# Kernel tuning notes

Measured on AMD Instinct MI355X. Metric: run time of the kernel, lower is better.

## Reference

```python
import jax, jax.numpy as jnp
import numpy as np

L, D_MODEL, D_INNER, DT_RANK, D_STATE, D_CONV, VOCAB = 4, 768, 1536, 48, 16, 4, 32000
B, S = 1, 1024


def rmsnorm(x, w, eps=1e-5):
    return x * jax.lax.rsqrt(jnp.mean(x * x, axis=-1, keepdims=True) + eps) * w


def causal_depthwise_conv(x, w, b):
    # x: [B,S,D]; w: [D,1,K] (torch Conv1d groups=D weight layout); causal left-pad K-1
    y = jax.lax.conv_general_dilated(
        x.transpose(0, 2, 1), w, window_strides=(1,), padding=[(D_CONV - 1, 0)],
        dimension_numbers=('NCH', 'OIH', 'NCH'), feature_group_count=D_INNER)
    return y.transpose(0, 2, 1) + b


def selective_scan(u, dt, A, Bm, Cm, Dv):
    # Faithful to the source: A_delta = exp(dt (x) A), clamp(min=-20) is a no-op on exp output
    A_delta = jnp.clip(jnp.exp(jnp.einsum('bld,dn->bldn', dt, A)), -20.0, None)
    B_delta_u = jnp.einsum('bld,bld,bln->bldn', dt, u, Bm)
    shifted = jnp.pad(A_delta[:, 1:], ((0, 0), (1, 0), (0, 0), (0, 0)))
    A_cum = jnp.exp(jnp.cumsum(shifted, axis=1))
    h = B_delta_u / (A_cum + 1e-12)
    y = jnp.einsum('bldn,bln->bld', jnp.cumsum(h, axis=1) * A_cum, Cm)
    return y + u * Dv


def setup_inputs() -> dict:
    key = jax.random.key(0)
    ks = jax.random.split(key, 8)
    return {
        'tokens': jax.random.randint(ks[0], (B, S), 0, VOCAB),
        'embedding': jax.random.normal(ks[1], (VOCAB, D_MODEL), jnp.float32) * 0.02,
        'norm_w': jnp.ones((L, D_MODEL), jnp.float32),
        'in_proj_w': jax.random.normal(ks[2], (L, 2 * D_INNER, D_MODEL), jnp.float32) * 0.02,
        'conv_w': jax.random.normal(ks[3], (L, D_INNER, 1, D_CONV), jnp.float32) * 0.2,
        'conv_b': jnp.zeros((L, D_INNER), jnp.float32),
        'x_proj_w': jax.random.normal(ks[4], (L, DT_RANK + 2 * D_STATE, D_INNER), jnp.float32) * 0.02,
        'dt_proj_w': jax.random.normal(ks[5], (L, D_INNER, DT_RANK), jnp.float32) * 0.001,
        'dt_proj_b': jnp.full((L, D_INNER), 5.0, jnp.float32),  # delta~5 keeps exp(cumsum(exp(dt*A))) finite
        'A_log': jnp.tile(jnp.log(jnp.arange(1, D_STATE + 1, dtype=jnp.float32)), (L, D_INNER, 1)),
        'D_skip': jnp.ones((L, D_INNER), jnp.float32),
        'out_proj_w': jax.random.normal(ks[6], (L, D_MODEL, D_INNER), jnp.float32) * 0.02,
        'final_norm_w': jnp.ones((D_MODEL,), jnp.float32),
    }


def reference(tokens, embedding, norm_w, in_proj_w, conv_w, conv_b, x_proj_w,
              dt_proj_w, dt_proj_b, A_log, D_skip, out_proj_w, final_norm_w):
    x = embedding[tokens]  # [B,S,d_model]
    for i in range(L):
        h = rmsnorm(x, norm_w[i])
        xz = h @ in_proj_w[i].T                      # [B,S,2*d_inner]
        xi, res = xz[..., :D_INNER], xz[..., D_INNER:]
        xi = jax.nn.silu(causal_depthwise_conv(xi, conv_w[i], conv_b[i]))
        proj = xi @ x_proj_w[i].T                    # [B,S,dt_rank+2*d_state]
        dt = jax.nn.softplus(proj[..., :DT_RANK] @ dt_proj_w[i].T + dt_proj_b[i])
        Bm = proj[..., DT_RANK:DT_RANK + D_STATE]
        Cm = proj[..., DT_RANK + D_STATE:]
        A = -jnp.exp(A_log[i])                       # [d_inner, d_state]
        y = selective_scan(xi, dt, A, Bm, Cm, D_skip[i])
        x = x + (y * jax.nn.silu(res)) @ out_proj_w[i].T
    return rmsnorm(x, final_norm_w) @ embedding.T    # tied LM head: [B,S,vocab]
```

## Files before the change

### kernel.cpp

```cpp
#include <hip/hip_runtime.h>
#include <hip/hip_bf16.h>
#include <cmath>

namespace {

constexpr int kL      = 4;
constexpr int kDModel = 768;
constexpr int kDInner = 1536;
constexpr int kDtRank = 48;
constexpr int kDState = 16;
constexpr int kDConv  = 4;
constexpr int kSeq    = 1024;
constexpr int kPLd    = 96;
constexpr int kPB     = 128;
constexpr int kVocab  = 32000;
constexpr int kCH     = 64;
constexpr int kNCH    = kSeq / kCH;
constexpr int kDN     = kDInner * kDState;
constexpr int kSplitIn  = 4;
constexpr int kSplitOut = 8;

using short8 = __attribute__((ext_vector_type(8))) short;
using f32x4  = __attribute__((ext_vector_type(4))) float;

__device__ __forceinline__ float silu_f(float v) {
    return v / (1.f + __expf(-v));
}

__device__ __forceinline__ unsigned short f2bu(float v) {
    __hip_bfloat16 h = __float2bfloat16(v);
    return *reinterpret_cast<unsigned short*>(&h);
}

__device__ __forceinline__ void split_bf16(float v, __hip_bfloat16& hi, __hip_bfloat16& lo) {
    hi = __float2bfloat16(v);
    lo = __float2bfloat16(v - __bfloat162float(hi));
}

__device__ __forceinline__ void split_u(float v, unsigned short& hi, unsigned short& lo) {
    __hip_bfloat16 h, l;
    split_bf16(v, h, l);
    hi = *reinterpret_cast<unsigned short*>(&h);
    lo = *reinterpret_cast<unsigned short*>(&l);
}

__global__ void __launch_bounds__(256) f2b_kernel(
    const float* __restrict__ src, __hip_bfloat16* __restrict__ dst, int n) {
    int i = (blockIdx.x * 256 + threadIdx.x) * 8;
    const int stride = gridDim.x * 256 * 8;
    for (; i + 7 < n; i += stride) {
        const float4 a = *reinterpret_cast<const float4*>(src + i);
        const float4 b = *reinterpret_cast<const float4*>(src + i + 4);
        union { unsigned short u[8]; uint4 v; } pk;
        pk.u[0] = f2bu(a.x); pk.u[1] = f2bu(a.y); pk.u[2] = f2bu(a.z); pk.u[3] = f2bu(a.w);
        pk.u[4] = f2bu(b.x); pk.u[5] = f2bu(b.y); pk.u[6] = f2bu(b.z); pk.u[7] = f2bu(b.w);
        *reinterpret_cast<uint4*>(reinterpret_cast<unsigned short*>(dst) + i) = pk.v;
    }
}

__global__ void __launch_bounds__(256) split3_kernel(
    const float* __restrict__ src, int rows, int cols,
    __hip_bfloat16* __restrict__ dst) {
    const int idx = blockIdx.x * 256 + threadIdx.x;
    const int c4cnt = cols >> 2;
    if (idx >= rows * c4cnt) return;
    const int r = idx / c4cnt, c = (idx % c4cnt) << 2;
    const float4 v = *reinterpret_cast<const float4*>(src + (size_t)r * cols + c);
    ushort4 hi4, lo4;
    split_u(v.x, hi4.x, lo4.x); split_u(v.y, hi4.y, lo4.y);
    split_u(v.z, hi4.z, lo4.z); split_u(v.w, hi4.w, lo4.w);
    unsigned short* row = reinterpret_cast<unsigned short*>(dst) + (size_t)r * 3 * cols;
    *reinterpret_cast<ushort4*>(row + c) = hi4;
    *reinterpret_cast<ushort4*>(row + cols + c) = hi4;
    *reinterpret_cast<ushort4*>(row + 2 * cols + c) = lo4;
}

__global__ void __launch_bounds__(256) dup2_kernel(
    const float* __restrict__ src, __hip_bfloat16* __restrict__ dst,
    int rows, int cols) {
    const int idx = blockIdx.x * 256 + threadIdx.x;
    const int c4cnt = cols >> 2;
    if (idx >= rows * c4cnt) return;
    const int r = idx / c4cnt, c = (idx % c4cnt) << 2;
    const float4 v = *reinterpret_cast<const float4*>(src + (size_t)r * cols + c);
    ushort4 hi4 = {f2bu(v.x), f2bu(v.y), f2bu(v.z), f2bu(v.w)};
    unsigned short* row = reinterpret_cast<unsigned short*>(dst) + (size_t)r * 2 * cols;
    *reinterpret_cast<ushort4*>(row + c) = hi4;
    *reinterpret_cast<ushort4*>(row + cols + c) = hi4;
}

__global__ void __launch_bounds__(256) split3x_kernel(
    const float* __restrict__ src, __hip_bfloat16* __restrict__ dst) {
    const int idx = blockIdx.x * 256 + threadIdx.x;
    constexpr int c4cnt = kDInner >> 2;
    if (idx >= kL * kPB * c4cnt) return;
    const int layer = idx / (kPB * c4cnt);
    const int rem   = idx % (kPB * c4cnt);
    const int r = rem / c4cnt, c = (rem % c4cnt) << 2;
    float4 v = {0.f, 0.f, 0.f, 0.f};
    if (r < kDtRank + 2 * kDState)
        v = *reinterpret_cast<const float4*>(
            src + (size_t)layer * (kDtRank + 2 * kDState) * kDInner + (size_t)r * kDInner + c);
    ushort4 hi4, lo4;
    split_u(v.x, hi4.x, lo4.x); split_u(v.y, hi4.y, lo4.y);
    split_u(v.z, hi4.z, lo4.z); split_u(v.w, hi4.w, lo4.w);
    unsigned short* row = reinterpret_cast<unsigned short*>(dst)
        + ((size_t)layer * kPB + r) * 3 * kDInner;
    *reinterpret_cast<ushort4*>(row + c) = hi4;
    *reinterpret_cast<ushort4*>(row + kDInner + c) = hi4;
    *reinterpret_cast<ushort4*>(row + 2 * kDInner + c) = lo4;
}

__global__ void __launch_bounds__(256) embed_rms_kernel(
    const int* __restrict__ tokens, const float* __restrict__ emb,
    const float* __restrict__ w, float* __restrict__ x,
    __hip_bfloat16* __restrict__ h2) {
    const int s = blockIdx.x;
    const int t = tokens[s];
    const float* src = emb + (size_t)t * kDModel;
    float v[3];
    float ss = 0.f;
    #pragma unroll
    for (int j = 0; j < 3; ++j) {
        const int d = threadIdx.x + j * 256;
        v[j] = src[d];
        x[(size_t)s * kDModel + d] = v[j];
        ss = fmaf(v[j], v[j], ss);
    }
    #pragma unroll
    for (int m = 32; m; m >>= 1) ss += __shfl_xor(ss, m);
    __shared__ float red[4];
    if ((threadIdx.x & 63) == 0) red[threadIdx.x >> 6] = ss;
    __syncthreads();
    const float total = red[0] + red[1] + red[2] + red[3];
    const float scale = rsqrtf(total / (float)kDModel + 1e-5f);
    __hip_bfloat16* dst = h2 + (size_t)s * 3 * kDModel;
    #pragma unroll
    for (int j = 0; j < 3; ++j) {
        const int d = threadIdx.x + j * 256;
        const float hv = v[j] * scale * w[d];
        __hip_bfloat16 hi, lo;
        split_bf16(hv, hi, lo);
        dst[d] = hi; dst[kDModel + d] = lo; dst[2 * kDModel + d] = hi;
    }
}

template <bool FINAL>
__global__ void __launch_bounds__(256) reduce_rms_kernel(
    const float* __restrict__ parts, size_t stride,
    const float* __restrict__ w, float* __restrict__ x,
    __hip_bfloat16* __restrict__ out) {
    const int s = blockIdx.x;
    float v[3];
    float ss = 0.f;
    #pragma unroll
    for (int j = 0; j < 3; ++j) {
        const int d = threadIdx.x + j * 256;
        const size_t off = (size_t)s * kDModel + d;
        float acc = x[off];
        #pragma unroll
        for (int p = 0; p < kSplitOut; ++p) acc += parts[(size_t)p * stride + off];
        v[j] = acc;
        x[off] = acc;
        ss = fmaf(acc, acc, ss);
    }
    #pragma unroll
    for (int m = 32; m; m >>= 1) ss += __shfl_xor(ss, m);
    __shared__ float red[4];
    if ((threadIdx.x & 63) == 0) red[threadIdx.x >> 6] = ss;
    __syncthreads();
    const float total = red[0] + red[1] + red[2] + red[3];
    const float scale = rsqrtf(total / (float)kDModel + 1e-5f);
    #pragma unroll
    for (int j = 0; j < 3; ++j) {
        const int d = threadIdx.x + j * 256;
        const float hv = v[j] * scale * w[d];
        if (FINAL) {
            out[(size_t)s * kDModel + d] = __float2bfloat16(hv);
        } else {
            __hip_bfloat16 hi, lo;
            split_bf16(hv, hi, lo);
            __hip_bfloat16* dst = out + (size_t)s * 3 * kDModel;
            dst[d] = hi; dst[kDModel + d] = lo; dst[2 * kDModel + d] = hi;
        }
    }
}

template <int BM, int BN, int KSPLIT>
__global__ void __launch_bounds__(256) mfma_gemm(
    const __hip_bfloat16* __restrict__ A, int lda,
    const __hip_bfloat16* __restrict__ B, int ldb,
    float* __restrict__ C, int ldc,
    int N, int K, size_t partStride) {
    constexpr int BK = 32;
    static_assert(BM == 128 && BN == 128, "staging assumes 128x128");
    __shared__ unsigned short As[2][BM * BK];
    __shared__ unsigned short Bs[2][BN * BK];
    const int tid  = threadIdx.x;
    const int lane = tid & 63;

    const int nwg = gridDim.x * gridDim.y;
    int bid = blockIdx.y * gridDim.x + blockIdx.x;
    {
        const int q = nwg >> 3, r = nwg & 7;
        const int xcd = bid & 7, pos = bid >> 3;
        bid = (xcd < r ? xcd * (q + 1) : r * (q + 1) + (xcd - r) * q) + pos;
    }
    const int m0 = (bid % gridDim.x) * BM;
    const int n0 = (bid / gridDim.x) * BN;

    const int Kp = K / KSPLIT;
    const int kbeg = (KSPLIT > 1) ? blockIdx.z * Kp : 0;
    float* Cw = (KSPLIT > 1) ? C + (size_t)blockIdx.z * partStride : C;
    constexpr int WM = BM / 2, WN = BN / 2;
    constexpr int MR = WM / 16, NR = WN / 16;
    const int wave = tid >> 6;
    const int wm = (wave >> 1) * WM, wn = (wave & 1) * WN;
    const int l15 = lane & 15, l4 = lane >> 4;
    f32x4 acc[MR][NR] = {};

    auto stage = [&](int buf, int k0) {
        #pragma unroll
        for (int i = 0; i < 2; ++i) {
            const int idx = tid + i * 256;
            const int r = idx >> 2, qv = idx & 3;
            const int qs = qv ^ ((r >> 1) & 3);
            __builtin_amdgcn_global_load_lds(
                (const __attribute__((address_space(1))) void*)(A + (size_t)(m0 + r) * lda + k0 + qs * 8),
                (__attribute__((address_space(3))) void*)(&As[buf][(idx - lane) * 8]),
                16, 0, 0);
        }
        #pragma unroll
        for (int i = 0; i < 2; ++i) {
            const int idx = tid + i * 256;
            const int r = idx >> 2, qv = idx & 3;
            const int qs = qv ^ ((r >> 1) & 3);
            __builtin_amdgcn_global_load_lds(
                (const __attribute__((address_space(1))) void*)(B + (size_t)(n0 + r) * ldb + k0 + qs * 8),
                (__attribute__((address_space(3))) void*)(&Bs[buf][(idx - lane) * 8]),
                16, 0, 0);
        }
    };

    const int nt = Kp / BK;
    int cur = 0;
    stage(0, kbeg);
    for (int t = 0; t < nt; ++t) {
        if (t + 1 < nt) {
            stage(cur ^ 1, kbeg + (t + 1) * BK);
            asm volatile("s_waitcnt vmcnt(4)" ::: "memory");
        } else {
            asm volatile("s_waitcnt vmcnt(0)" ::: "memory");
        }
        __builtin_amdgcn_s_barrier();

        short8 af[MR], bfv[NR];
        #pragma unroll
        for (int mi = 0; mi < MR; ++mi) {
            const int R = wm + mi * 16 + l15;
            af[mi] = *reinterpret_cast<const short8*>(&As[cur][(R * 4 + (l4 ^ ((R >> 1) & 3))) * 8]);
        }
        #pragma unroll
        for (int ni = 0; ni < NR; ++ni) {
            const int R = wn + ni * 16 + l15;
            bfv[ni] = *reinterpret_cast<const short8*>(&Bs[cur][(R * 4 + (l4 ^ ((R >> 1) & 3))) * 8]);
        }
        #pragma unroll
        for (int mi = 0; mi < MR; ++mi)
            #pragma unroll
            for (int ni = 0; ni < NR; ++ni)
                acc[mi][ni] = __builtin_amdgcn_mfma_f32_16x16x32_bf16(
                    af[mi], bfv[ni], acc[mi][ni], 0, 0, 0);

        asm volatile("s_waitcnt lgkmcnt(0)" ::: "memory");
        __builtin_amdgcn_s_barrier();
        cur ^= 1;
    }

    #pragma unroll
    for (int mi = 0; mi < MR; ++mi) {
        const int mrow = m0 + wm + mi * 16 + l4 * 4;
        #pragma unroll
        for (int ni = 0; ni < NR; ++ni) {
            const int ncol = n0 + wn + ni * 16 + l15;
            if (ncol >= N) continue;
            #pragma unroll
            for (int r = 0; r < 4; ++r)
                Cw[(size_t)(mrow + r) * ldc + ncol] = acc[mi][ni][r];
        }
    }
}

template <int NP>
__global__ void __launch_bounds__(256) reduce_parts(
    const float* __restrict__ parts, size_t stride,
    float* __restrict__ dst, int count) {
    const int i = (blockIdx.x * 256 + threadIdx.x) * 4;
    if (i >= count) return;
    float4 s = *reinterpret_cast<const float4*>(parts + i);
    #pragma unroll
    for (int p = 1; p < NP; ++p) {
        const float4 v = *reinterpret_cast<const float4*>(parts + (size_t)p * stride + i);
        s.x += v.x; s.y += v.y; s.z += v.z; s.w += v.w;
    }
    *reinterpret_cast<float4*>(dst + i) = s;
}

__global__ void __launch_bounds__(256) conv_silu_kernel(
    const float* __restrict__ parts, size_t stride,
    const float* __restrict__ cw, const float* __restrict__ cb,
    float* __restrict__ xi, __hip_bfloat16* __restrict__ xi2) {
    const int s = blockIdx.x;
    const int d = blockIdx.y * 256 + threadIdx.x;
    float acc = cb[d];
    #pragma unroll
    for (int k = 0; k < kDConv; ++k) {
        const int sl = s - (kDConv - 1) + k;
        if (sl >= 0) {
            const size_t off = (size_t)sl * (2 * kDInner) + d;
            float xzv = parts[off];
            #pragma unroll
            for (int p = 1; p < kSplitIn; ++p) xzv += parts[(size_t)p * stride + off];
            acc = fmaf(xzv, cw[d * kDConv + k], acc);
        }
    }
    const float v = silu_f(acc);
    xi[(size_t)s * kDInner + d] = v;
    __hip_bfloat16 hi, lo;
    split_bf16(v, hi, lo);
    __hip_bfloat16* row = xi2 + (size_t)s * 3 * kDInner;
    row[d] = hi; row[kDInner + d] = lo; row[2 * kDInner + d] = hi;
}


__device__ __forceinline__ void compute_dt_tile(
    const float* __restrict__ proj, const float* __restrict__ dtw,
    const float* __restrict__ dtb, int l0, int d0, int tid,
    float (*sP)[kDtRank], float (*sdtw)[kDtRank + 1], float (*sdt)[16]) {
    for (int idx = tid; idx < kCH * kDtRank; idx += 256) {
        const int r = idx / kDtRank, c = idx % kDtRank;
        sP[r][c] = proj[(size_t)(l0 + r) * kPLd + c];
    }
    for (int idx = tid; idx < 16 * kDtRank; idx += 256) {
        const int dd = idx / kDtRank, c = idx % kDtRank;
        sdtw[dd][c] = dtw[(size_t)(d0 + dd) * kDtRank + c];
    }
    __syncthreads();
    #pragma unroll
    for (int e = 0; e < 4; ++e) {
        const int idx = tid + e * 256;
        const int r = idx >> 4, dd = idx & 15;
        float acc = dtb[d0 + dd];
        #pragma unroll
        for (int k = 0; k < kDtRank; ++k)
            acc = fmaf(sP[r][k], sdtw[dd][k], acc);
        acc = (acc > 20.f) ? acc : log1pf(__expf(acc));
        sdt[r][dd] = acc;
    }
}

__global__ void __launch_bounds__(256) scan_part1(
    const float* __restrict__ u, const float* __restrict__ proj,
    const float* __restrict__ A_log, const float* __restrict__ dtw,
    const float* __restrict__ dtb,
    float* __restrict__ P, float* __restrict__ S) {
    __shared__ float sP[kCH][kDtRank];
    __shared__ float sdtw[16][kDtRank + 1];
    __shared__ float sdt[kCH][16], su[kCH][16], sB[kCH][16];
    const int tid = threadIdx.x;
    const int n = tid & 15, dl = tid >> 4;
    const int d0 = blockIdx.x * 16;
    const int l0 = blockIdx.y * kCH;
    for (int idx = tid; idx < kCH * 16; idx += 256) {
        const int r = idx >> 4, c = idx & 15;
        su[r][c] = u[(size_t)(l0 + r) * kDInner + d0 + c];
        sB[r][c] = proj[(size_t)(l0 + r) * kPLd + kDtRank + c];
    }
    compute_dt_tile(proj, dtw, dtb, l0, d0, tid, sP, sdtw, sdt);
    __syncthreads();
    const int d = d0 + dl;
    const float Adn = -__expf(A_log[d * kDState + n]);
    float state = 0.f, sumA = 0.f;
    #pragma unroll 8
    for (int l = 0; l < kCH; ++l) {
        const float dtv = sdt[l][dl];
        const float adelta = __expf(dtv * Adn);
        const float mult = __expf(adelta);
        state = fmaf(state, mult, dtv * su[l][dl] * sB[l][n]);
        sumA += adelta;
    }
    const int dn = d * kDState + n;
    P[(size_t)blockIdx.y * kDN + dn] = __expf(sumA);
    S[(size_t)blockIdx.y * kDN + dn] = state;
}

__global__ void __launch_bounds__(256) scan_part2(
    const float* __restrict__ u, const float* __restrict__ proj,
    const float* __restrict__ A_log, const float* __restrict__ dtw,
    const float* __restrict__ dtb, const float* __restrict__ D_skip,
    const float* __restrict__ P, const float* __restrict__ S,
    const float* __restrict__ resparts, size_t rstride,
    __hip_bfloat16* __restrict__ g2) {
    __shared__ float sP[kCH][kDtRank];
    __shared__ float sdtw[16][kDtRank + 1];
    __shared__ float sdt[kCH][16], su[kCH][16], sB[kCH][16], sC[kCH][16];
    __shared__ float sy[kCH][16];
    const int tid = threadIdx.x;
    const int n = tid & 15, dl = tid >> 4;
    const int d0 = blockIdx.x * 16;
    const int l0 = blockIdx.y * kCH;
    for (int idx = tid; idx < kCH * 16; idx += 256) {
        const int r = idx >> 4, c = idx & 15;
        su[r][c] = u[(size_t)(l0 + r) * kDInner + d0 + c];
        sB[r][c] = proj[(size_t)(l0 + r) * kPLd + kDtRank + c];
        sC[r][c] = proj[(size_t)(l0 + r) * kPLd + kDtRank + kDState + c];
    }
    compute_dt_tile(proj, dtw, dtb, l0, d0, tid, sP, sdtw, sdt);
    const int dn = d0 * kDState + tid;
    float state = 0.f;
    for (int jj = 0; jj < (int)blockIdx.y; ++jj) {
        const size_t idx = (size_t)jj * kDN + dn;
        state = fmaf(state, P[idx], S[idx]);
    }
    __syncthreads();
    const int d = d0 + dl;
    const float Adn = -__expf(A_log[d * kDState + n]);
    const float Dv  = D_skip[d];
    for (int l = 0; l < kCH; ++l) {
        const float dtv = sdt[l][dl];
        const float uv  = su[l][dl];
        const float mult = __expf(__expf(dtv * Adn));
        state = fmaf(state, mult, dtv * uv * sB[l][n]);
        float contrib = state * sC[l][n];
        contrib += __shfl_xor(contrib, 8);
        contrib += __shfl_xor(contrib, 4);
        contrib += __shfl_xor(contrib, 2);
        contrib += __shfl_xor(contrib, 1);
        if (n == 0) sy[l][dl] = fmaf(uv, Dv, contrib);
    }
    __syncthreads();
    for (int idx = tid; idx < kCH * 16; idx += 256) {
        const int r = idx >> 4, c = idx & 15;
        const size_t roff = (size_t)(l0 + r) * (2 * kDInner) + kDInner + d0 + c;
        float res = resparts[roff];
        #pragma unroll
        for (int p = 1; p < kSplitIn; ++p) res += resparts[(size_t)p * rstride + roff];
        const float v = sy[r][c] * silu_f(res);
        __hip_bfloat16 hi, lo;
        split_bf16(v, hi, lo);
        __hip_bfloat16* row = g2 + (size_t)(l0 + r) * 2 * kDInner;
        row[d0 + c] = hi; row[kDInner + d0 + c] = lo;
    }
}

}

extern "C" void kernel_launch(void* const* d_in, const int* in_sizes, int n_in,
                              void* d_out, int out_size, void* d_ws, size_t ws_size,
                              hipStream_t stream) {
    const int*   tokens       = (const int*)d_in[0];
    const float* embedding    = (const float*)d_in[1];
    const float* norm_w       = (const float*)d_in[2];
    const float* in_proj_w    = (const float*)d_in[3];
    const float* conv_w       = (const float*)d_in[4];
    const float* conv_b       = (const float*)d_in[5];
    const float* x_proj_w     = (const float*)d_in[6];
    const float* dt_proj_w    = (const float*)d_in[7];
    const float* dt_proj_b    = (const float*)d_in[8];
    const float* A_log        = (const float*)d_in[9];
    const float* D_skip       = (const float*)d_in[10];
    const float* out_proj_w   = (const float*)d_in[11];
    const float* final_norm_w = (const float*)d_in[12];
    float* out = (float*)d_out;

    constexpr int K3m = 3 * kDModel;
    constexpr int K3i = 3 * kDInner;
    constexpr int K2i = 2 * kDInner;

    char* ws = (char*)d_ws;
    auto alloc = [&](size_t bytes) { char* p = ws; ws += (bytes + 255) & ~(size_t)255; return p; };
    float* x    = (float*)alloc((size_t)kSeq * kDModel * 4);
    float* xi   = (float*)alloc((size_t)kSeq * kDInner * 4);
    float* proj = (float*)alloc((size_t)kSeq * kPLd * 4);
    float* scanP  = (float*)alloc((size_t)kNCH * kDN * 4);
    float* scanS  = (float*)alloc((size_t)kNCH * kDN * 4);
    float* partsXZ = (float*)alloc((size_t)kSplitIn * kSeq * 2 * kDInner * 4);
    float* partsP  = (float*)alloc((size_t)24 * kSeq * kPLd * 4);
    float* partsO  = (float*)alloc((size_t)kSplitOut * kSeq * kDModel * 4);
    __hip_bfloat16* h_bf   = (__hip_bfloat16*)alloc((size_t)kSeq * kDModel * 2);
    __hip_bfloat16* h2     = (__hip_bfloat16*)alloc((size_t)kSeq * K3m * 2);
    __hip_bfloat16* xi2    = (__hip_bfloat16*)alloc((size_t)kSeq * K3i * 2);
    __hip_bfloat16* g2     = (__hip_bfloat16*)alloc((size_t)kSeq * K2i * 2);
    __hip_bfloat16* emb_bf = (__hip_bfloat16*)alloc((size_t)kVocab * kDModel * 2);
    __hip_bfloat16* inw2   = (__hip_bfloat16*)alloc((size_t)kL * 2 * kDInner * K3m * 2);
    __hip_bfloat16* outw2  = (__hip_bfloat16*)alloc((size_t)kL * kDModel * K2i * 2);
    __hip_bfloat16* xw2    = (__hip_bfloat16*)alloc((size_t)kL * kPB * K3i * 2);

    f2b_kernel<<<4096, 256, 0, stream>>>(embedding, emb_bf, kVocab * kDModel);
    dup2_kernel<<<(kL * kDModel * kDInner / 4 + 255) / 256, 256, 0, stream>>>(
        out_proj_w, outw2, kL * kDModel, kDInner);
    split3_kernel<<<(kL * 2 * kDInner * kDModel / 4 + 255) / 256, 256, 0, stream>>>(
        in_proj_w, kL * 2 * kDInner, kDModel, inw2);
    split3x_kernel<<<(kL * kPB * kDInner / 4 + 255) / 256, 256, 0, stream>>>(
        x_proj_w, xw2);

    embed_rms_kernel<<<kSeq, 256, 0, stream>>>(tokens, embedding, norm_w, x, h2);

    for (int i = 0; i < kL; ++i) {
        mfma_gemm<128, 128, kSplitIn><<<dim3(kSeq / 128, 2 * kDInner / 128, kSplitIn), 256, 0, stream>>>(
            h2, K3m, inw2 + (size_t)i * 2 * kDInner * K3m, K3m,
            partsXZ, 2 * kDInner, 2 * kDInner, K3m, (size_t)kSeq * 2 * kDInner);

        conv_silu_kernel<<<dim3(kSeq, kDInner / 256), 256, 0, stream>>>(
            partsXZ, (size_t)kSeq * 2 * kDInner,
            conv_w + (size_t)i * kDInner * kDConv, conv_b + (size_t)i * kDInner,
            xi, xi2);

        mfma_gemm<128, 128, 24><<<dim3(kSeq / 128, 1, 24), 256, 0, stream>>>(
            xi2, K3i, xw2 + (size_t)i * kPB * K3i, K3i,
            partsP, kPLd, kPLd, K3i, (size_t)kSeq * kPLd);
        reduce_parts<24><<<(kSeq * kPLd / 4 + 255) / 256, 256, 0, stream>>>(
            partsP, (size_t)kSeq * kPLd, proj, kSeq * kPLd);

        const float* A_l  = A_log + (size_t)i * kDInner * kDState;
        const float* dtw  = dt_proj_w + (size_t)i * kDInner * kDtRank;
        const float* dtb  = dt_proj_b + (size_t)i * kDInner;
        scan_part1<<<dim3(kDInner / 16, kNCH), 256, 0, stream>>>(
            xi, proj, A_l, dtw, dtb, scanP, scanS);
        scan_part2<<<dim3(kDInner / 16, kNCH), 256, 0, stream>>>(
            xi, proj, A_l, dtw, dtb, D_skip + (size_t)i * kDInner,
            scanP, scanS, partsXZ, (size_t)kSeq * 2 * kDInner, g2);

        mfma_gemm<128, 128, kSplitOut><<<dim3(kSeq / 128, kDModel / 128, kSplitOut), 256, 0, stream>>>(
            g2, K2i, outw2 + (size_t)i * kDModel * K2i, K2i,
            partsO, kDModel, kDModel, K2i, (size_t)kSeq * kDModel);

        if (i + 1 < kL) {
            reduce_rms_kernel<false><<<kSeq, 256, 0, stream>>>(
                partsO, (size_t)kSeq * kDModel, norm_w + (size_t)(i + 1) * kDModel, x, h2);
        } else {
            reduce_rms_kernel<true><<<kSeq, 256, 0, stream>>>(
                partsO, (size_t)kSeq * kDModel, final_norm_w, x, h_bf);
        }
    }

    mfma_gemm<128, 128, 1><<<dim3(kSeq / 128, kVocab / 128, 1), 256, 0, stream>>>(
        h_bf, kDModel, emb_bf, kDModel, out, kVocab, kVocab, kDModel, 0);
}
```

Before: 767.6 us.

## Add dedicated 256x256 MFMA kernel for the vocab LM-head GEMM

Replaces the generic 128x128 MFMA GEMM for the final 1024x32000x768 LM-head projection with a specialised 256x256-tile, 512-thread kernel. It stages A and B into LDS with direct global-to-LDS loads, an XOR swizzle and double buffering, and interleaves fragment loads with MFMA quadrants under raised wave priority. Workgroup IDs are remapped so that tiles are grouped per XCD for better L2 locality. The larger tiles cut the global traffic per FLOP, but they need 128 KB of dynamic LDS and 128 accumulator floats per thread, which limits occupancy to one block per CU.

```diff
diff --git a/kernel.cpp b/kernel.cpp
--- a/kernel.cpp
+++ b/kernel.cpp
@@ -291,6 +291,129 @@
     }
 }
 
+__global__ void __launch_bounds__(512) vocab_gemm(
+    const __hip_bfloat16* __restrict__ A,
+    const __hip_bfloat16* __restrict__ B,
+    float* __restrict__ C) {
+    constexpr int BM = 256, BN = 256, BK = 64;
+    constexpr int K = kDModel, NT = K / BK;
+    constexpr int lda = kDModel, ldb = kDModel, ldc = kVocab;
+    extern __shared__ unsigned short lds[];
+    unsigned short* AsB = lds;
+    unsigned short* BsB = lds + 2 * BM * BK;
+    const int tid = threadIdx.x, lane = tid & 63;
+    const int wave = tid >> 6;
+    const int wr = wave >> 2;
+    const int wc = wave & 3;
+    const int l15 = lane & 15, l4 = lane >> 4;
+
+    const int nwg = gridDim.x * gridDim.y;
+    int bid = blockIdx.y * gridDim.x + blockIdx.x;
+    {
+        const int q = nwg >> 3, r = nwg & 7;
+        const int xcd = bid & 7, pos = bid >> 3;
+        bid = (xcd < r ? xcd * (q + 1) : r * (q + 1) + (xcd - r) * q) + pos;
+    }
+    const int m0 = (bid % gridDim.x) * BM;
+    const int n0 = (bid / gridDim.x) * BN;
+
+    f32x4 acc[8][4] = {};
+
+    auto stage = [&](int buf, int k0) {
+        #pragma unroll
+        for (int i = 0; i < 4; ++i) {
+            const int idx = tid + i * 512;
+            const int r = idx >> 3, p = idx & 7;
+            const int ps = p ^ (r & 7);
+            __builtin_amdgcn_global_load_lds(
+                (const __attribute__((address_space(1))) void*)(A + (size_t)(m0 + r) * lda + k0 + ps * 8),
+                (__attribute__((address_space(3))) void*)(AsB + (size_t)buf * BM * BK + (size_t)(idx - lane) * 8),
+                16, 0, 0);
+        }
+        #pragma unroll
+        for (int i = 0; i < 4; ++i) {
+            const int idx = tid + i * 512;
+            const int r = idx >> 3, p = idx & 7;
+            const int ps = p ^ (r & 7);
+            __builtin_amdgcn_global_load_lds(
+                (const __attribute__((address_space(1))) void*)(B + (size_t)(n0 + r) * ldb + k0 + ps * 8),
+                (__attribute__((address_space(3))) void*)(BsB + (size_t)buf * BN * BK + (size_t)(idx - lane) * 8),
+                16, 0, 0);
+        }
+    };
+
+    stage(0, 0);
+    for (int t = 0; t < NT; ++t) {
+        asm volatile("s_waitcnt vmcnt(0)" ::: "memory");
+        __builtin_amdgcn_s_barrier();
+        if (t + 1 < NT) stage((t + 1) & 1, (t + 1) * BK);
+        const unsigned short* Ab = AsB + (size_t)(t & 1) * BM * BK;
+        const unsigned short* Bb = BsB + (size_t)(t & 1) * BN * BK;
+
+        short8 af[4][2], bfv[2][2];
+
+#define LOAD_A(MQ)                                                          \
+        _Pragma("unroll")                                                   \
+        for (int mi = 0; mi < 4; ++mi) {                                    \
+            _Pragma("unroll")                                               \
+            for (int kk = 0; kk < 2; ++kk) {                                \
+                const int R = wr * 128 + (MQ) * 64 + mi * 16 + l15;         \
+                const int ps = (kk * 4 + l4) ^ (R & 7);                     \
+                af[mi][kk] = *reinterpret_cast<const short8*>(              \
+                    Ab + ((size_t)R * 8 + ps) * 8);                         \
+            }                                                               \
+        }
+#define LOAD_B(NQ)                                                          \
+        _Pragma("unroll")                                                   \
+        for (int ni = 0; ni < 2; ++ni) {                                    \
+            _Pragma("unroll")                                               \
+            for (int kk = 0; kk < 2; ++kk) {                                \
+                const int R = wc * 64 + (NQ) * 32 + ni * 16 + l15;          \
+                const int ps = (kk * 4 + l4) ^ (R & 7);                     \
+                bfv[ni][kk] = *reinterpret_cast<const short8*>(             \
+                    Bb + ((size_t)R * 8 + ps) * 8);                         \
+            }                                                               \
+        }
+#define QUAD(MQ, NQ)                                                        \
+        __builtin_amdgcn_s_setprio(1);                                      \
+        _Pragma("unroll")                                                   \
+        for (int mi = 0; mi < 4; ++mi)                                      \
+            _Pragma("unroll")                                               \
+            for (int ni = 0; ni < 2; ++ni)                                  \
+                _Pragma("unroll")                                           \
+                for (int kk = 0; kk < 2; ++kk)                              \
+                    acc[(MQ) * 4 + mi][(NQ) * 2 + ni] =                     \
+                        __builtin_amdgcn_mfma_f32_16x16x32_bf16(            \
+                            af[mi][kk], bfv[ni][kk],                        \
+                            acc[(MQ) * 4 + mi][(NQ) * 2 + ni], 0, 0, 0);    \
+        __builtin_amdgcn_s_setprio(0);
+
+        LOAD_A(0); LOAD_B(0);
+        QUAD(0, 0);
+        LOAD_B(1);
+        QUAD(0, 1);
+        LOAD_A(1);
+        QUAD(1, 1);
+        LOAD_B(0);
+        QUAD(1, 0);
+#undef LOAD_A
+#undef LOAD_B
+#undef QUAD
+    }
+
+    #pragma unroll
+    for (int mg = 0; mg < 8; ++mg) {
+        const int mrow = m0 + wr * 128 + mg * 16 + l4 * 4;
+        #pragma unroll
+        for (int ng = 0; ng < 4; ++ng) {
+            const int ncol = n0 + wc * 64 + ng * 16 + l15;
+            #pragma unroll
+            for (int r = 0; r < 4; ++r)
+                C[(size_t)(mrow + r) * ldc + ncol] = acc[mg][ng][r];
+        }
+    }
+}
+
 template <int NP>
 __global__ void __launch_bounds__(256) reduce_parts(
     const float* __restrict__ parts, size_t stride,
@@ -331,7 +454,6 @@
     __hip_bfloat16* row = xi2 + (size_t)s * 3 * kDInner;
     row[d] = hi; row[kDInner + d] = lo; row[2 * kDInner + d] = hi;
 }
-
 
 __device__ __forceinline__ void compute_dt_tile(
     const float* __restrict__ proj, const float* __restrict__ dtw,
@@ -477,6 +599,9 @@
     constexpr int K3i = 3 * kDInner;
     constexpr int K2i = 2 * kDInner;
 
+    (void)hipFuncSetAttribute((const void*)vocab_gemm,
+                              hipFuncAttributeMaxDynamicSharedMemorySize, 131072);
+
     char* ws = (char*)d_ws;
     auto alloc = [&](size_t bytes) { char* p = ws; ws += (bytes + 255) & ~(size_t)255; return p; };
     float* x    = (float*)alloc((size_t)kSeq * kDModel * 4);
@@ -544,6 +669,6 @@
         }
     }
 
-    mfma_gemm<128, 128, 1><<<dim3(kSeq / 128, kVocab / 128, 1), 256, 0, stream>>>(
-        h_bf, kDModel, emb_bf, kDModel, out, kVocab, kVocab, kDModel, 0);
-}
+    vocab_gemm<<<dim3(kSeq / 256, kVocab / 256), 512, 131072, stream>>>(
+        h_bf, emb_bf, out);
+}
```

Measured after the change: 746.1 us. 2.8% less time.

## Merge prep kernels into one launch and add large-tile LM-head GEMM

Applied to the files above, without the earlier changes.

Merges the five preprocessing kernels (embedding bf16 cast, weight duplicate/split, and embed+RMSnorm) into one prep_kernel that dispatches on block index, removing four launches. Replaces the generic 128x128 vocab projection with a dedicated 512x256-tile, 512-thread GEMM. The new GEMM uses triple-buffered global_load_lds staging with XOR swizzling, XCD-aware block remapping and raised wave priority around the MFMAs. Larger tiles cut redundant operand traffic for the biggest GEMM. The cost is heavy register use (64 accumulators per lane), 144KB of LDS, and only 250 workgroups, which may underfill the GPU.

```diff
diff --git a/kernel.cpp b/kernel.cpp
--- a/kernel.cpp
+++ b/kernel.cpp
@@ -20,6 +20,13 @@
 constexpr int kSplitIn  = 4;
 constexpr int kSplitOut = 8;
 
+constexpr int kPrepEmbed   = kSeq;
+constexpr int kPrepF2b     = kVocab * kDModel / (8 * 256);
+constexpr int kPrepDup2    = kL * kDModel * (kDInner / 4) / 256;
+constexpr int kPrepSplit3  = kL * 2 * kDInner * (kDModel / 4) / 256;
+constexpr int kPrepSplit3x = kL * kPB * (kDInner / 4) / 256;
+constexpr int kPrepBlocks  = kPrepEmbed + kPrepF2b + kPrepDup2 + kPrepSplit3 + kPrepSplit3x;
+
 using short8 = __attribute__((ext_vector_type(8))) short;
 using f32x4  = __attribute__((ext_vector_type(4))) float;
 
@@ -44,104 +51,108 @@
     lo = *reinterpret_cast<unsigned short*>(&l);
 }
 
-__global__ void __launch_bounds__(256) f2b_kernel(
-    const float* __restrict__ src, __hip_bfloat16* __restrict__ dst, int n) {
-    int i = (blockIdx.x * 256 + threadIdx.x) * 8;
-    const int stride = gridDim.x * 256 * 8;
-    for (; i + 7 < n; i += stride) {
-        const float4 a = *reinterpret_cast<const float4*>(src + i);
-        const float4 b = *reinterpret_cast<const float4*>(src + i + 4);
+__global__ void __launch_bounds__(256) prep_kernel(
+    const int* __restrict__ tokens, const float* __restrict__ embedding,
+    const float* __restrict__ norm_w, const float* __restrict__ in_proj_w,
+    const float* __restrict__ out_proj_w, const float* __restrict__ x_proj_w,
+    float* __restrict__ x, __hip_bfloat16* __restrict__ h2,
+    __hip_bfloat16* __restrict__ emb_bf, __hip_bfloat16* __restrict__ inw2,
+    __hip_bfloat16* __restrict__ outw2, __hip_bfloat16* __restrict__ xw2) {
+    const int tid = threadIdx.x;
+    int b = blockIdx.x;
+
+    if (b < kPrepEmbed) {
+        const int s = b;
+        const int t = tokens[s];
+        const float* src = embedding + (size_t)t * kDModel;
+        float v[3];
+        float ss = 0.f;
+        #pragma unroll
+        for (int j = 0; j < 3; ++j) {
+            const int d = tid + j * 256;
+            v[j] = src[d];
+            x[(size_t)s * kDModel + d] = v[j];
+            ss = fmaf(v[j], v[j], ss);
+        }
+        #pragma unroll
+        for (int m = 32; m; m >>= 1) ss += __shfl_xor(ss, m);
+        __shared__ float red[4];
+        if ((tid & 63) == 0) red[tid >> 6] = ss;
+        __syncthreads();
+        const float total = red[0] + red[1] + red[2] + red[3];
+        const float scale = rsqrtf(total / (float)kDModel + 1e-5f);
+        __hip_bfloat16* dst = h2 + (size_t)s * 3 * kDModel;
+        #pragma unroll
+        for (int j = 0; j < 3; ++j) {
+            const int d = tid + j * 256;
+            const float hv = v[j] * scale * norm_w[d];
+            __hip_bfloat16 hi, lo;
+            split_bf16(hv, hi, lo);
+            dst[d] = hi; dst[kDModel + d] = lo; dst[2 * kDModel + d] = hi;
+        }
+        return;
+    }
+    b -= kPrepEmbed;
+
+    if (b < kPrepF2b) {
+        const int i = (b * 256 + tid) * 8;
+        const float4 a = *reinterpret_cast<const float4*>(embedding + i);
+        const float4 c = *reinterpret_cast<const float4*>(embedding + i + 4);
         union { unsigned short u[8]; uint4 v; } pk;
         pk.u[0] = f2bu(a.x); pk.u[1] = f2bu(a.y); pk.u[2] = f2bu(a.z); pk.u[3] = f2bu(a.w);
-        pk.u[4] = f2bu(b.x); pk.u[5] = f2bu(b.y); pk.u[6] = f2bu(b.z); pk.u[7] = f2bu(b.w);
-        *reinterpret_cast<uint4*>(reinterpret_cast<unsigned short*>(dst) + i) = pk.v;
-    }
-}
-
-__global__ void __launch_bounds__(256) split3_kernel(
-    const float* __restrict__ src, int rows, int cols,
-    __hip_bfloat16* __restrict__ dst) {
-    const int idx = blockIdx.x * 256 + threadIdx.x;
-    const int c4cnt = cols >> 2;
-    if (idx >= rows * c4cnt) return;
-    const int r = idx / c4cnt, c = (idx % c4cnt) << 2;
-    const float4 v = *reinterpret_cast<const float4*>(src + (size_t)r * cols + c);
-    ushort4 hi4, lo4;
-    split_u(v.x, hi4.x, lo4.x); split_u(v.y, hi4.y, lo4.y);
-    split_u(v.z, hi4.z, lo4.z); split_u(v.w, hi4.w, lo4.w);
-    unsigned short* row = reinterpret_cast<unsigned short*>(dst) + (size_t)r * 3 * cols;
-    *reinterpret_cast<ushort4*>(row + c) = hi4;
-    *reinterpret_cast<ushort4*>(row + cols + c) = hi4;
-    *reinterpret_cast<ushort4*>(row + 2 * cols + c) = lo4;
-}
-
-__global__ void __launch_bounds__(256) dup2_kernel(
-    const float* __restrict__ src, __hip_bfloat16* __restrict__ dst,
-    int rows, int cols) {
-    const int idx = blockIdx.x * 256 + threadIdx.x;
-    const int c4cnt = cols >> 2;
-    if (idx >= rows * c4cnt) return;
-    const int r = idx / c4cnt, c = (idx % c4cnt) << 2;
-    const float4 v = *reinterpret_cast<const float4*>(src + (size_t)r * cols + c);
-    ushort4 hi4 = {f2bu(v.x), f2bu(v.y), f2bu(v.z), f2bu(v.w)};
-    unsigned short* row = reinterpret_cast<unsigned short*>(dst) + (size_t)r * 2 * cols;
-    *reinterpret_cast<ushort4*>(row + c) = hi4;
-    *reinterpret_cast<ushort4*>(row + cols + c) = hi4;
-}
-
-__global__ void __launch_bounds__(256) split3x_kernel(
-    const float* __restrict__ src, __hip_bfloat16* __restrict__ dst) {
-    const int idx = blockIdx.x * 256 + threadIdx.x;
-    constexpr int c4cnt = kDInner >> 2;
-    if (idx >= kL * kPB * c4cnt) return;
-    const int layer = idx / (kPB * c4cnt);
-    const int rem   = idx % (kPB * c4cnt);
-    const int r = rem / c4cnt, c = (rem % c4cnt) << 2;
-    float4 v = {0.f, 0.f, 0.f, 0.f};
-    if (r < kDtRank + 2 * kDState)
-        v = *reinterpret_cast<const float4*>(
-            src + (size_t)layer * (kDtRank + 2 * kDState) * kDInner + (size_t)r * kDInner + c);
-    ushort4 hi4, lo4;
-    split_u(v.x, hi4.x, lo4.x); split_u(v.y, hi4.y, lo4.y);
-    split_u(v.z, hi4.z, lo4.z); split_u(v.w, hi4.w, lo4.w);
-    unsigned short* row = reinterpret_cast<unsigned short*>(dst)
-        + ((size_t)layer * kPB + r) * 3 * kDInner;
-    *reinterpret_cast<ushort4*>(row + c) = hi4;
-    *reinterpret_cast<ushort4*>(row + kDInner + c) = hi4;
-    *reinterpret_cast<ushort4*>(row + 2 * kDInner + c) = lo4;
-}
-
-__global__ void __launch_bounds__(256) embed_rms_kernel(
-    const int* __restrict__ tokens, const float* __restrict__ emb,
-    const float* __restrict__ w, float* __restrict__ x,
-    __hip_bfloat16* __restrict__ h2) {
-    const int s = blockIdx.x;
-    const int t = tokens[s];
-    const float* src = emb + (size_t)t * kDModel;
-    float v[3];
-    float ss = 0.f;
-    #pragma unroll
-    for (int j = 0; j < 3; ++j) {
-        const int d = threadIdx.x + j * 256;
-        v[j] = src[d];
-        x[(size_t)s * kDModel + d] = v[j];
-        ss = fmaf(v[j], v[j], ss);
-    }
-    #pragma unroll
-    for (int m = 32; m; m >>= 1) ss += __shfl_xor(ss, m);
-    __shared__ float red[4];
-    if ((threadIdx.x & 63) == 0) red[threadIdx.x >> 6] = ss;
-    __syncthreads();
-    const float total = red[0] + red[1] + red[2] + red[3];
-    const float scale = rsqrtf(total / (float)kDModel + 1e-5f);
-    __hip_bfloat16* dst = h2 + (size_t)s * 3 * kDModel;
-    #pragma unroll
-    for (int j = 0; j < 3; ++j) {
-        const int d = threadIdx.x + j * 256;
-        const float hv = v[j] * scale * w[d];
-        __hip_bfloat16 hi, lo;
-        split_bf16(hv, hi, lo);
-        dst[d] = hi; dst[kDModel + d] = lo; dst[2 * kDModel + d] = hi;
+        pk.u[4] = f2bu(c.x); pk.u[5] = f2bu(c.y); pk.u[6] = f2bu(c.z); pk.u[7] = f2bu(c.w);
+        *reinterpret_cast<uint4*>(reinterpret_cast<unsigned short*>(emb_bf) + i) = pk.v;
+        return;
+    }
+    b -= kPrepF2b;
+
+    if (b < kPrepDup2) {
+        const int idx = b * 256 + tid;
+        constexpr int cols = kDInner, c4cnt = kDInner / 4;
+        const int r = idx / c4cnt, c = (idx % c4cnt) << 2;
+        const float4 v = *reinterpret_cast<const float4*>(out_proj_w + (size_t)r * cols + c);
+        ushort4 hi4 = {f2bu(v.x), f2bu(v.y), f2bu(v.z), f2bu(v.w)};
+        unsigned short* row = reinterpret_cast<unsigned short*>(outw2) + (size_t)r * 2 * cols;
+        *reinterpret_cast<ushort4*>(row + c) = hi4;
+        *reinterpret_cast<ushort4*>(row + cols + c) = hi4;
+        return;
+    }
+    b -= kPrepDup2;
+
+    if (b < kPrepSplit3) {
+        const int idx = b * 256 + tid;
+        constexpr int cols = kDModel, c4cnt = kDModel / 4;
+        const int r = idx / c4cnt, c = (idx % c4cnt) << 2;
+        const float4 v = *reinterpret_cast<const float4*>(in_proj_w + (size_t)r * cols + c);
+        ushort4 hi4, lo4;
+        split_u(v.x, hi4.x, lo4.x); split_u(v.y, hi4.y, lo4.y);
+        split_u(v.z, hi4.z, lo4.z); split_u(v.w, hi4.w, lo4.w);
+        unsigned short* row = reinterpret_cast<unsigned short*>(inw2) + (size_t)r * 3 * cols;
+        *reinterpret_cast<ushort4*>(row + c) = hi4;
+        *reinterpret_cast<ushort4*>(row + cols + c) = hi4;
+        *reinterpret_cast<ushort4*>(row + 2 * cols + c) = lo4;
+        return;
+    }
+    b -= kPrepSplit3;
+
+    {
+        const int idx = b * 256 + tid;
+        constexpr int c4cnt = kDInner / 4;
+        const int layer = idx / (kPB * c4cnt);
+        const int rem   = idx % (kPB * c4cnt);
+        const int r = rem / c4cnt, c = (rem % c4cnt) << 2;
+        float4 v = {0.f, 0.f, 0.f, 0.f};
+        if (r < kDtRank + 2 * kDState)
+            v = *reinterpret_cast<const float4*>(
+                x_proj_w + (size_t)layer * (kDtRank + 2 * kDState) * kDInner + (size_t)r * kDInner + c);
+        ushort4 hi4, lo4;
+        split_u(v.x, hi4.x, lo4.x); split_u(v.y, hi4.y, lo4.y);
+        split_u(v.z, hi4.z, lo4.z); split_u(v.w, hi4.w, lo4.w);
+        unsigned short* row = reinterpret_cast<unsigned short*>(xw2)
+            + ((size_t)layer * kPB + r) * 3 * kDInner;
+        *reinterpret_cast<ushort4*>(row + c) = hi4;
+        *reinterpret_cast<ushort4*>(row + kDInner + c) = hi4;
+        *reinterpret_cast<ushort4*>(row + 2 * kDInner + c) = lo4;
     }
 }
 
@@ -291,6 +302,108 @@
     }
 }
 
+__global__ void __launch_bounds__(512) vocab_gemm(
+    const __hip_bfloat16* __restrict__ A,
+    const __hip_bfloat16* __restrict__ B,
+    float* __restrict__ C) {
+    constexpr int BM = 512, BN = 256, BK = 32;
+    constexpr int K = kDModel, NT = K / BK;
+    constexpr int lda = kDModel, ldb = kDModel, ldc = kVocab;
+    constexpr int ASZ = BM * BK;
+    constexpr int BSZ = BN * BK;
+    extern __shared__ unsigned short lds[];
+    unsigned short* AsB = lds;
+    unsigned short* BsB = lds + 3 * ASZ;
+    const int tid = threadIdx.x, lane = tid & 63;
+    const int wave = tid >> 6;
+    const int wr = wave >> 1;
+    const int wc = wave & 1;
+    const int l15 = lane & 15, l4 = lane >> 4;
+
+    const int nwg = gridDim.x * gridDim.y;
+    int bid = blockIdx.y * gridDim.x + blockIdx.x;
+    {
+        const int q = nwg >> 3, r = nwg & 7;
+        const int xcd = bid & 7, pos = bid >> 3;
+        bid = (xcd < r ? xcd * (q + 1) : r * (q + 1) + (xcd - r) * q) + pos;
+    }
+    const int m0 = (bid % gridDim.x) * BM;
+    const int n0 = (bid / gridDim.x) * BN;
+
+    f32x4 acc[8][8] = {};
+
+    auto stage = [&](int buf, int k0) {
+        #pragma unroll
+        for (int i = 0; i < 4; ++i) {
+            const int idx = tid + i * 512;
+            const int r = idx >> 2, p = idx & 3;
+            const int ps = p ^ ((r >> 1) & 3);
+            __builtin_amdgcn_global_load_lds(
+                (const __attribute__((address_space(1))) void*)(A + (size_t)(m0 + r) * lda + k0 + ps * 8),
+                (__attribute__((address_space(3))) void*)(AsB + (size_t)buf * ASZ + (size_t)(idx - lane) * 8),
+                16, 0, 0);
+        }
+        #pragma unroll
+        for (int i = 0; i < 2; ++i) {
+            const int idx = tid + i * 512;
+            const int r = idx >> 2, p = idx & 3;
+            const int ps = p ^ ((r >> 1) & 3);
+            __builtin_amdgcn_global_load_lds(
+                (const __attribute__((address_space(1))) void*)(B + (size_t)(n0 + r) * ldb + k0 + ps * 8),
+                (__attribute__((address_space(3))) void*)(BsB + (size_t)buf * BSZ + (size_t)(idx - lane) * 8),
+                16, 0, 0);
+        }
+    };
+
+    stage(0, 0);
+    stage(1, BK);
+    int cur = 0;
+    for (int t = 0; t < NT; ++t) {
+        if (t + 1 < NT) asm volatile("s_waitcnt vmcnt(6)" ::: "memory");
+        else            asm volatile("s_waitcnt vmcnt(0)" ::: "memory");
+        __builtin_amdgcn_s_barrier();
+        if (t + 2 < NT) stage((t + 2) % 3, (t + 2) * BK);
+
+        const unsigned short* Ab = AsB + (size_t)cur * ASZ;
+        const unsigned short* Bb = BsB + (size_t)cur * BSZ;
+
+        short8 af[8], bfv[8];
+        #pragma unroll
+        for (int mi = 0; mi < 8; ++mi) {
+            const int R = wr * 128 + mi * 16 + l15;
+            const int p = l4 ^ ((R >> 1) & 3);
+            af[mi] = *reinterpret_cast<const short8*>(Ab + ((size_t)R * 4 + p) * 8);
+        }
+        #pragma unroll
+        for (int ni = 0; ni < 8; ++ni) {
+            const int R = wc * 128 + ni * 16 + l15;
+            const int p = l4 ^ ((R >> 1) & 3);
+            bfv[ni] = *reinterpret_cast<const short8*>(Bb + ((size_t)R * 4 + p) * 8);
+        }
+        __builtin_amdgcn_s_setprio(1);
+        #pragma unroll
+        for (int mi = 0; mi < 8; ++mi)
+            #pragma unroll
+            for (int ni = 0; ni < 8; ++ni)
+                acc[mi][ni] = __builtin_amdgcn_mfma_f32_16x16x32_bf16(
+                    af[mi], bfv[ni], acc[mi][ni], 0, 0, 0);
+        __builtin_amdgcn_s_setprio(0);
+        cur = (cur + 1) % 3;
+    }
+
+    #pragma unroll
+    for (int mg = 0; mg < 8; ++mg) {
+        const int mrow = m0 + wr * 128 + mg * 16 + l4 * 4;
+        #pragma unroll
+        for (int ng = 0; ng < 8; ++ng) {
+            const int ncol = n0 + wc * 128 + ng * 16 + l15;
+            #pragma unroll
+            for (int r = 0; r < 4; ++r)
+                C[(size_t)(mrow + r) * ldc + ncol] = acc[mg][ng][r];
+        }
+    }
+}
+
 template <int NP>
 __global__ void __launch_bounds__(256) reduce_parts(
     const float* __restrict__ parts, size_t stride,
@@ -331,7 +444,6 @@
     __hip_bfloat16* row = xi2 + (size_t)s * 3 * kDInner;
     row[d] = hi; row[kDInner + d] = lo; row[2 * kDInner + d] = hi;
 }
-
 
 __device__ __forceinline__ void compute_dt_tile(
     const float* __restrict__ proj, const float* __restrict__ dtw,
@@ -477,6 +589,9 @@
     constexpr int K3i = 3 * kDInner;
     constexpr int K2i = 2 * kDInner;
 
+    (void)hipFuncSetAttribute((const void*)vocab_gemm,
+                              hipFuncAttributeMaxDynamicSharedMemorySize, 147456);
+
     char* ws = (char*)d_ws;
     auto alloc = [&](size_t bytes) { char* p = ws; ws += (bytes + 255) & ~(size_t)255; return p; };
     float* x    = (float*)alloc((size_t)kSeq * kDModel * 4);
@@ -496,15 +611,9 @@
     __hip_bfloat16* outw2  = (__hip_bfloat16*)alloc((size_t)kL * kDModel * K2i * 2);
     __hip_bfloat16* xw2    = (__hip_bfloat16*)alloc((size_t)kL * kPB * K3i * 2);
 
-    f2b_kernel<<<4096, 256, 0, stream>>>(embedding, emb_bf, kVocab * kDModel);
-    dup2_kernel<<<(kL * kDModel * kDInner / 4 + 255) / 256, 256, 0, stream>>>(
-        out_proj_w, outw2, kL * kDModel, kDInner);
-    split3_kernel<<<(kL * 2 * kDInner * kDModel / 4 + 255) / 256, 256, 0, stream>>>(
-        in_proj_w, kL * 2 * kDInner, kDModel, inw2);
-    split3x_kernel<<<(kL * kPB * kDInner / 4 + 255) / 256, 256, 0, stream>>>(
-        x_proj_w, xw2);
-
-    embed_rms_kernel<<<kSeq, 256, 0, stream>>>(tokens, embedding, norm_w, x, h2);
+    prep_kernel<<<kPrepBlocks, 256, 0, stream>>>(
+        tokens, embedding, norm_w, in_proj_w, out_proj_w, x_proj_w,
+        x, h2, emb_bf, inw2, outw2, xw2);
 
     for (int i = 0; i < kL; ++i) {
         mfma_gemm<128, 128, kSplitIn><<<dim3(kSeq / 128, 2 * kDInner / 128, kSplitIn), 256, 0, stream>>>(
@@ -544,6 +653,6 @@
         }
     }
 
-    mfma_gemm<128, 128, 1><<<dim3(kSeq / 128, kVocab / 128, 1), 256, 0, stream>>>(
-        h_bf, kDModel, emb_bf, kDModel, out, kVocab, kVocab, kDModel, 0);
-}
+    vocab_gemm<<<dim3(kSeq / 512, kVocab / 256), 512, 147456, stream>>>(
+        h_bf, emb_bf, out);
+}
```

Measured after the change: 1.033 ms. 1.35x slower.
